# Kernel optimization log

Measured on AMD Instinct MI355X. Metric: run time of the kernel, lower is better.

Reference implementation:

```python
import jax, jax.numpy as jnp
import numpy as np

N, E, D, L, G = 10000, 320000, 256, 5, 128
RWSE, DEG_V = 16, 1001
BN_EPS = 1e-5


def setup_inputs() -> dict:
    key = jax.random.key(0)
    ks = jax.random.split(key, 12)
    s = 1.0 / np.sqrt(D)
    return {
        'feat_id': jax.random.randint(ks[0], (N,), 0, 100000, dtype=jnp.int64 if jax.config.jax_enable_x64 else jnp.int32),
        'edge_index': jax.random.randint(ks[1], (2, E), 0, N),
        'batch_idx': jnp.sort(jax.random.randint(ks[2], (N,), 0, G)),
        'rwse': jax.random.normal(ks[3], (N, RWSE), jnp.float32),
        'in_degrees': jax.random.randint(ks[4], (N,), 0, DEG_V),
        # value_projection: Linear(fixed_input_dim=D -> D); stored as [in, out]
        'w_val': jax.random.normal(ks[5], (D, D), jnp.float32) * s,
        'b_val': jnp.zeros((D,), jnp.float32),
        # rwse_projection: Linear(RWSE -> D)
        'w_rwse': jax.random.normal(ks[6], (RWSE, D), jnp.float32) * (1.0 / np.sqrt(RWSE)),
        'b_rwse': jnp.zeros((D,), jnp.float32),
        # degree_embedding table (clamped to [0, 1000])
        'deg_emb': jax.random.normal(ks[7], (DEG_V, D), jnp.float32) * 0.02,
        # per-layer GIN MLP: Linear-ReLU-Linear, stacked over L layers
        'mlp_w1': jax.random.normal(ks[8], (L, D, D), jnp.float32) * s,
        'mlp_b1': jnp.zeros((L, D), jnp.float32),
        'mlp_w2': jax.random.normal(ks[9], (L, D, D), jnp.float32) * s,
        'mlp_b2': jnp.zeros((L, D), jnp.float32),
        # BatchNorm1d (eval mode: running stats)
        'bn_gamma': jnp.ones((L, D), jnp.float32),
        'bn_beta': jnp.zeros((L, D), jnp.float32),
        'bn_mean': jnp.zeros((L, D), jnp.float32),
        'bn_var': jax.random.uniform(ks[10], (L, D), jnp.float32, 0.5, 1.5),
        # GIN eps per layer
        'eps_gin': jnp.zeros((L,), jnp.float32),
    }


def reference(feat_id, edge_index, batch_idx, rwse, in_degrees,
              w_val, b_val, w_rwse, b_rwse, deg_emb,
              mlp_w1, mlp_b1, mlp_w2, mlp_b2,
              bn_gamma, bn_beta, bn_mean, bn_var, eps_gin):
    # --- node feature embedding ---
    h_id = jnp.remainder(feat_id, D)
    h_one = jax.nn.one_hot(h_id, D, dtype=jnp.float32)            # [N, D]
    h = h_one @ w_val + b_val + rwse @ w_rwse + b_rwse            # value + rwse projections
    deg = jnp.clip(in_degrees, 0, 1000)
    h = h + deg_emb[deg]                                          # degree embedding

    src, dst = edge_index[0], edge_index[1]
    for l in range(L):
        # GIN message passing: sum neighbor features into dst (gather -> scatter-add)
        agg = jax.ops.segment_sum(h[src], dst, num_segments=N)    # [N, D]
        y = agg + (1.0 + eps_gin[l]) * h
        # MLP (Linear-ReLU-Linear)
        y = jax.nn.relu(y @ mlp_w1[l] + mlp_b1[l]) @ mlp_w2[l] + mlp_b2[l]
        # BatchNorm1d (eval: running stats) + ReLU
        y = (y - bn_mean[l]) * (bn_gamma[l] * jax.lax.rsqrt(bn_var[l] + BN_EPS)) + bn_beta[l]
        h = jax.nn.relu(y)

    # --- mean pooling per graph ---
    sums = jax.ops.segment_sum(h, batch_idx, num_segments=G)                     # [G, D]
    cnt = jax.ops.segment_sum(jnp.ones((N, 1), h.dtype), batch_idx, num_segments=G)
    graph_feature = sums / jnp.maximum(cnt, 1.0)
    return graph_feature, h
```

## Files before the change

kernel.cpp:

```cpp
#include <hip/hip_runtime.h>
#include <hip/hip_bf16.h>

#define N_NODES 10000
#define N_EDGES 320000
#define DIM     256
#define N_LAYERS 5
#define N_GRAPHS 128
#define RWSE_K  16
#define GBM 16

typedef __bf16 bf16_t;
typedef bf16_t bf16x8 __attribute__((ext_vector_type(8)));
typedef float  f32x4  __attribute__((ext_vector_type(4)));

__device__ inline ushort f2bf(float f) {
    union { float f; unsigned u; } v; v.f = f;
    unsigned r = v.u + 0x7fff + ((v.u >> 16) & 1);
    return (ushort)(r >> 16);
}
__device__ inline float bfbits2f(unsigned hi16) {
    union { unsigned u; float f; } v; v.u = hi16;
    return v.f;
}

__global__ __launch_bounds__(256)
void setup_kernel(const int* __restrict__ feat_id,
                  const float* __restrict__ rwse,
                  const int* __restrict__ in_deg,
                  const float* __restrict__ w_val,
                  const float* __restrict__ b_val,
                  const float* __restrict__ w_rwse,
                  const float* __restrict__ b_rwse,
                  const float* __restrict__ deg_emb,
                  ushort* __restrict__ hb,
                  const int* __restrict__ ei, int* __restrict__ cnt_arr,
                  const float* __restrict__ w1, const float* __restrict__ w2,
                  ushort* __restrict__ wt1, ushort* __restrict__ wt2,
                  const float* __restrict__ gamma, const float* __restrict__ beta,
                  const float* __restrict__ mean, const float* __restrict__ var,
                  const float* __restrict__ b2, float* __restrict__ scale,
                  float* __restrict__ shift) {
    __shared__ float r[RWSE_K];
    __shared__ float t[32][33];
    int b = blockIdx.x;
    int tid = threadIdx.x;
    if (b < N_NODES) {
        int i = b, d = tid;
        if (d < RWSE_K) r[d] = rwse[i * RWSE_K + d];
        __syncthreads();
        int hid = feat_id[i] & (DIM - 1);
        int dg = in_deg[i];
        dg = dg < 0 ? 0 : (dg > 1000 ? 1000 : dg);
        float v = w_val[hid * DIM + d] + b_val[d] + b_rwse[d] + deg_emb[dg * DIM + d];
#pragma unroll
        for (int k = 0; k < RWSE_K; ++k) v += r[k] * w_rwse[k * DIM + d];
        hb[i * DIM + d] = f2bf(v);
    } else if (b < 11250) {
        int e = (b - N_NODES) * 256 + tid;
        if (e < N_EDGES) atomicAdd(&cnt_arr[ei[N_EDGES + e]], 1);
    } else if (b < 11890) {
        int w_id = b - 11250;
        int l = w_id >> 7;
        int rem = w_id & 127;
        int mat = rem >> 6;
        int tile = rem & 63;
        const float* W  = (mat ? w2  : w1)  + (size_t)l * DIM * DIM;
        ushort*      Wt = (mat ? wt2 : wt1) + (size_t)l * DIM * DIM;
        int k0 = (tile >> 3) * 32, n0 = (tile & 7) * 32;
        int tx = tid & 31, ty = tid >> 5;
#pragma unroll
        for (int j = 0; j < 4; ++j)
            t[ty + j * 8][tx] = W[(k0 + ty + j * 8) * DIM + n0 + tx];
        __syncthreads();
#pragma unroll
        for (int j = 0; j < 4; ++j)
            Wt[(n0 + ty + j * 8) * DIM + k0 + tx] = f2bf(t[tx][ty + j * 8]);
    } else {
        int l = b - 11890;
        int idx = l * DIM + tid;
        float s = gamma[idx] * rsqrtf(var[idx] + 1e-5f);
        scale[idx] = s;
        shift[idx] = beta[idx] + (b2[idx] - mean[idx]) * s;
    }
}

__global__ __launch_bounds__(1024)
void scan_kernel(const int* __restrict__ cnt_arr, int* __restrict__ cur, int n) {
    __shared__ int wsum[16];
    __shared__ int carry_sh;
    int tid = threadIdx.x, wave = tid >> 6, lane = tid & 63;
    if (tid == 0) carry_sh = 0;
    __syncthreads();
    for (int base = 0; base < n; base += 1024) {
        int idx = base + tid;
        int v = (idx < n) ? cnt_arr[idx] : 0;
        int s = v;
#pragma unroll
        for (int off = 1; off < 64; off <<= 1) {
            int t = __shfl_up(s, off, 64);
            if (lane >= off) s += t;
        }
        if (lane == 63) wsum[wave] = s;
        __syncthreads();
        if (wave == 0) {
            int ws = (lane < 16) ? wsum[lane] : 0;
#pragma unroll
            for (int off = 1; off < 16; off <<= 1) {
                int t = __shfl_up(ws, off, 64);
                if (lane >= off) ws += t;
            }
            if (lane < 16) wsum[lane] = ws;
        }
        __syncthreads();
        int excl = s - v + (wave ? wsum[wave - 1] : 0) + carry_sh;
        if (idx < n) cur[idx] = excl;
        __syncthreads();
        if (tid == 0) carry_sh += wsum[15];
        __syncthreads();
    }
}

__global__ __launch_bounds__(256)
void fill_kernel(const int* __restrict__ ei, int* __restrict__ cur,
                 int* __restrict__ cs) {
    int e = blockIdx.x * 256 + threadIdx.x;
    if (e < N_EDGES) {
        int d = ei[N_EDGES + e];
        int p = atomicAdd(&cur[d], 1);
        cs[p] = ei[e];
    }
}

#define ACCV(v)                                                        \
    acc[0] += bfbits2f((v).x << 16); acc[1] += bfbits2f((v).x & 0xffff0000u); \
    acc[2] += bfbits2f((v).y << 16); acc[3] += bfbits2f((v).y & 0xffff0000u); \
    acc[4] += bfbits2f((v).z << 16); acc[5] += bfbits2f((v).z & 0xffff0000u); \
    acc[6] += bfbits2f((v).w << 16); acc[7] += bfbits2f((v).w & 0xffff0000u);

__global__ __launch_bounds__(256)
void layer_kernel(const ushort* __restrict__ hb_in,
                  const int* __restrict__ cur, const int* __restrict__ cs,
                  const float* __restrict__ eps_gin, int layer,
                  const ushort* __restrict__ Wt1, const float* __restrict__ b1,
                  const ushort* __restrict__ Wt2,
                  const float* __restrict__ bnsc, const float* __restrict__ bnsh,
                  float* __restrict__ outF, ushort* __restrict__ outB) {
    __shared__ __align__(16) ushort As[GBM][DIM + 8];
    __shared__ __align__(16) ushort Bs[DIM][40];
    __shared__ __align__(16) ushort Ts[GBM][DIM + 8];
    int tx = threadIdx.x;
    int row0 = blockIdx.x * GBM;
    int wave = tx >> 6, lane = tx & 63, quad = lane >> 4, l16 = lane & 15;
    int half = lane >> 5, sl = lane & 31;
    int wc = wave * 64;
    int srow = tx >> 2;
    int skol = (tx & 3) * 8;
    const uint4* hb4 = (const uint4*)hb_in;
    float sc = 1.0f + eps_gin[layer];

#pragma unroll
    for (int n = 0; n < 4; ++n) {
        int r = wave * 4 + n;
        int i = row0 + r;
        float acc[8];
#pragma unroll
        for (int t = 0; t < 8; ++t) acc[t] = 0.f;
        int e0 = i ? cur[i - 1] : 0;
        int e1 = cur[i];
        for (int base = e0; base < e1; base += 64) {
            int rem = e1 - base;
            int cnt = rem < 64 ? rem : 64;
            int idx = (base + lane < e1) ? cs[base + lane] : 0;
            int j = 0;
            for (; j + 8 <= cnt; j += 8) {
                int s0 = __shfl(idx, j + half, 64);
                int s1 = __shfl(idx, j + 2 + half, 64);
                int s2 = __shfl(idx, j + 4 + half, 64);
                int s3 = __shfl(idx, j + 6 + half, 64);
                uint4 v0 = hb4[(size_t)s0 * 32 + sl];
                uint4 v1 = hb4[(size_t)s1 * 32 + sl];
                uint4 v2 = hb4[(size_t)s2 * 32 + sl];
                uint4 v3 = hb4[(size_t)s3 * 32 + sl];
                ACCV(v0); ACCV(v1); ACCV(v2); ACCV(v3);
            }
            for (; j + 2 <= cnt; j += 2) {
                int s = __shfl(idx, j + half, 64);
                uint4 v = hb4[(size_t)s * 32 + sl];
                ACCV(v);
            }
            if (j < cnt) {
                int s = __shfl(idx, j, 64);
                if (half == 0) {
                    uint4 v = hb4[(size_t)s * 32 + sl];
                    ACCV(v);
                }
            }
        }
#pragma unroll
        for (int t = 0; t < 8; ++t) acc[t] += __shfl_xor(acc[t], 32, 64);
        if (half == 0) {
            uint4 sv = hb4[(size_t)i * 32 + sl];
            acc[0] += bfbits2f(sv.x << 16) * sc; acc[1] += bfbits2f(sv.x & 0xffff0000u) * sc;
            acc[2] += bfbits2f(sv.y << 16) * sc; acc[3] += bfbits2f(sv.y & 0xffff0000u) * sc;
            acc[4] += bfbits2f(sv.z << 16) * sc; acc[5] += bfbits2f(sv.z & 0xffff0000u) * sc;
            acc[6] += bfbits2f(sv.w << 16) * sc; acc[7] += bfbits2f(sv.w & 0xffff0000u) * sc;
            uint4 o;
            o.x = (uint)f2bf(acc[0]) | ((uint)f2bf(acc[1]) << 16);
            o.y = (uint)f2bf(acc[2]) | ((uint)f2bf(acc[3]) << 16);
            o.z = (uint)f2bf(acc[4]) | ((uint)f2bf(acc[5]) << 16);
            o.w = (uint)f2bf(acc[6]) | ((uint)f2bf(acc[7]) << 16);
            *(uint4*)&As[r][sl * 8] = o;
        }
    }
    __syncthreads();

    f32x4 acc4[4];
#pragma unroll
    for (int t = 0; t < 4; ++t) acc4[t] = (f32x4){0.f, 0.f, 0.f, 0.f};
    for (int k0 = 0; k0 < DIM; k0 += 32) {
#pragma unroll
        for (int j = 0; j < 4; ++j) {
            int rr = srow + 64 * j;
            *(uint4*)&Bs[rr][skol] = *(const uint4*)&Wt1[(size_t)rr * DIM + k0 + skol];
        }
        __syncthreads();
        bf16x8 af = *(const bf16x8*)&As[l16][k0 + quad * 8];
#pragma unroll
        for (int tj = 0; tj < 4; ++tj) {
            bf16x8 bfv = *(const bf16x8*)&Bs[wc + tj * 16 + l16][quad * 8];
            acc4[tj] = __builtin_amdgcn_mfma_f32_16x16x32_bf16(af, bfv, acc4[tj], 0, 0, 0);
        }
        __syncthreads();
    }
#pragma unroll
    for (int tj = 0; tj < 4; ++tj) {
        int col = wc + tj * 16 + l16;
        float bias = b1[col];
#pragma unroll
        for (int r = 0; r < 4; ++r)
            Ts[quad * 4 + r][col] = f2bf(fmaxf(acc4[tj][r] + bias, 0.f));
    }
    __syncthreads();

#pragma unroll
    for (int t = 0; t < 4; ++t) acc4[t] = (f32x4){0.f, 0.f, 0.f, 0.f};
    for (int k0 = 0; k0 < DIM; k0 += 32) {
#pragma unroll
        for (int j = 0; j < 4; ++j) {
            int rr = srow + 64 * j;
            *(uint4*)&Bs[rr][skol] = *(const uint4*)&Wt2[(size_t)rr * DIM + k0 + skol];
        }
        __syncthreads();
        bf16x8 af = *(const bf16x8*)&Ts[l16][k0 + quad * 8];
#pragma unroll
        for (int tj = 0; tj < 4; ++tj) {
            bf16x8 bfv = *(const bf16x8*)&Bs[wc + tj * 16 + l16][quad * 8];
            acc4[tj] = __builtin_amdgcn_mfma_f32_16x16x32_bf16(af, bfv, acc4[tj], 0, 0, 0);
        }
        __syncthreads();
    }
#pragma unroll
    for (int tj = 0; tj < 4; ++tj) {
        int col = wc + tj * 16 + l16;
        float s = bnsc[col], sh = bnsh[col];
#pragma unroll
        for (int r = 0; r < 4; ++r) {
            int row = row0 + quad * 4 + r;
            float v = fmaxf(acc4[tj][r] * s + sh, 0.f);
            if (outF) outF[(size_t)row * DIM + col] = v;
            if (outB) outB[(size_t)row * DIM + col] = f2bf(v);
        }
    }
}

__global__ __launch_bounds__(256)
void pool_kernel(const float* __restrict__ hfin, const int* __restrict__ batch,
                 float* __restrict__ out) {
    int g = blockIdx.x;
    int d = threadIdx.x;
    int l = 0, r = N_NODES;
    while (l < r) { int m = (l + r) >> 1; if (batch[m] < g) l = m + 1; else r = m; }
    int lo = l;
    r = N_NODES;
    while (l < r) { int m = (l + r) >> 1; if (batch[m] < g + 1) l = m + 1; else r = m; }
    int hi = l;
    float a0 = 0.f, a1 = 0.f, a2 = 0.f, a3 = 0.f;
    int i = lo;
    for (; i + 4 <= hi; i += 4) {
        a0 += hfin[(size_t)i * DIM + d];
        a1 += hfin[(size_t)(i + 1) * DIM + d];
        a2 += hfin[(size_t)(i + 2) * DIM + d];
        a3 += hfin[(size_t)(i + 3) * DIM + d];
    }
    for (; i < hi; ++i) a0 += hfin[(size_t)i * DIM + d];
    float c = (float)(hi - lo);
    if (c < 1.f) c = 1.f;
    out[g * DIM + d] = ((a0 + a1) + (a2 + a3)) / c;
}

extern "C" void kernel_launch(void* const* d_in, const int* in_sizes, int n_in,
                              void* d_out, int out_size, void* d_ws, size_t ws_size,
                              hipStream_t stream) {
    const int*   feat_id  = (const int*)d_in[0];
    const int*   ei       = (const int*)d_in[1];
    const int*   batch    = (const int*)d_in[2];
    const float* rwse     = (const float*)d_in[3];
    const int*   in_deg   = (const int*)d_in[4];
    const float* w_val    = (const float*)d_in[5];
    const float* b_val    = (const float*)d_in[6];
    const float* w_rwse   = (const float*)d_in[7];
    const float* b_rwse   = (const float*)d_in[8];
    const float* deg_emb  = (const float*)d_in[9];
    const float* mlp_w1   = (const float*)d_in[10];
    const float* mlp_b1   = (const float*)d_in[11];
    const float* mlp_w2   = (const float*)d_in[12];
    const float* mlp_b2   = (const float*)d_in[13];
    const float* bn_gamma = (const float*)d_in[14];
    const float* bn_beta  = (const float*)d_in[15];
    const float* bn_mean  = (const float*)d_in[16];
    const float* bn_var   = (const float*)d_in[17];
    const float* eps_gin  = (const float*)d_in[18];

    float* out = (float*)d_out;
    float* out_h = out + N_GRAPHS * DIM;

    char* w = (char*)d_ws;
    ushort* hb0  = (ushort*)w;
    ushort* hb1  = hb0 + (size_t)N_NODES * DIM;
    ushort* wt1  = hb1 + (size_t)N_NODES * DIM;
    ushort* wt2  = wt1 + (size_t)N_LAYERS * DIM * DIM;
    int* cnt_arr = (int*)(wt2 + (size_t)N_LAYERS * DIM * DIM);
    int* cur     = cnt_arr + N_NODES;
    int* cs      = cur + N_NODES;
    float* bnsc  = (float*)(cs + N_EDGES);
    float* bnsh  = bnsc + N_LAYERS * DIM;

    hipMemsetAsync(cnt_arr, 0, N_NODES * sizeof(int), stream);

    setup_kernel<<<11895, 256, 0, stream>>>(
        feat_id, rwse, in_deg, w_val, b_val, w_rwse, b_rwse, deg_emb,
        hb0, ei, cnt_arr, mlp_w1, mlp_w2, wt1, wt2,
        bn_gamma, bn_beta, bn_mean, bn_var, mlp_b2, bnsc, bnsh);
    scan_kernel<<<1, 1024, 0, stream>>>(cnt_arr, cur, N_NODES);
    fill_kernel<<<(N_EDGES + 255) / 256, 256, 0, stream>>>(ei, cur, cs);

    int ggrid = N_NODES / GBM;
    for (int l = 0; l < N_LAYERS; ++l) {
        bool last = (l == N_LAYERS - 1);
        const ushort* hin = (l & 1) ? hb1 : hb0;
        ushort* hout = (l & 1) ? hb0 : hb1;
        layer_kernel<<<ggrid, 256, 0, stream>>>(
            hin, cur, cs, eps_gin, l,
            wt1 + (size_t)l * DIM * DIM, mlp_b1 + l * DIM,
            wt2 + (size_t)l * DIM * DIM, bnsc + l * DIM, bnsh + l * DIM,
            last ? out_h : nullptr, last ? nullptr : hout);
    }

    pool_kernel<<<N_GRAPHS, 256, 0, stream>>>(out_h, batch, out);
}
```

Measured before the change: 329.7 us.

## Use 512-thread blocks with two interleaved rows per wave in GIN layer gather

The layer kernel now runs with 512 threads (8 waves) per block of 16 rows. Each wave aggregates two destination rows, and the neighbour gathers for both rows are interleaved in one loop so more independent loads are in flight at once. The MFMA stage is split so each wave computes 32 output columns instead of 64, and weight tiles are staged with fewer loads per thread. This aims to hide gather latency and raise occupancy, at the cost of more complex tail handling and duplicated code paths for the two rows.

```diff
diff --git a/kernel.cpp b/kernel.cpp
--- a/kernel.cpp
+++ b/kernel.cpp
@@ -131,13 +131,38 @@
     }
 }
 
-#define ACCV(v)                                                        \
-    acc[0] += bfbits2f((v).x << 16); acc[1] += bfbits2f((v).x & 0xffff0000u); \
-    acc[2] += bfbits2f((v).y << 16); acc[3] += bfbits2f((v).y & 0xffff0000u); \
-    acc[4] += bfbits2f((v).z << 16); acc[5] += bfbits2f((v).z & 0xffff0000u); \
-    acc[6] += bfbits2f((v).w << 16); acc[7] += bfbits2f((v).w & 0xffff0000u);
-
-__global__ __launch_bounds__(256)
+#define ACCP(a, v)                                                        \
+    a[0] += bfbits2f((v).x << 16); a[1] += bfbits2f((v).x & 0xffff0000u); \
+    a[2] += bfbits2f((v).y << 16); a[3] += bfbits2f((v).y & 0xffff0000u); \
+    a[4] += bfbits2f((v).z << 16); a[5] += bfbits2f((v).z & 0xffff0000u); \
+    a[6] += bfbits2f((v).w << 16); a[7] += bfbits2f((v).w & 0xffff0000u);
+
+#define SOLO8(idx, j, cnt, a)                                   \
+    for (; j + 8 <= cnt; j += 8) {                              \
+        int s0 = __shfl(idx, j + half, 64);                     \
+        int s1 = __shfl(idx, j + 2 + half, 64);                 \
+        int s2 = __shfl(idx, j + 4 + half, 64);                 \
+        int s3 = __shfl(idx, j + 6 + half, 64);                 \
+        uint4 v0 = hb4[(size_t)s0 * 32 + sl];                   \
+        uint4 v1 = hb4[(size_t)s1 * 32 + sl];                   \
+        uint4 v2 = hb4[(size_t)s2 * 32 + sl];                   \
+        uint4 v3 = hb4[(size_t)s3 * 32 + sl];                   \
+        ACCP(a, v0); ACCP(a, v1); ACCP(a, v2); ACCP(a, v3);     \
+    }                                                           \
+    for (; j + 2 <= cnt; j += 2) {                              \
+        int s = __shfl(idx, j + half, 64);                      \
+        uint4 v = hb4[(size_t)s * 32 + sl];                     \
+        ACCP(a, v);                                             \
+    }                                                           \
+    if (j < cnt) {                                              \
+        int s = __shfl(idx, j, 64);                             \
+        if (half == 0) {                                        \
+            uint4 v = hb4[(size_t)s * 32 + sl];                 \
+            ACCP(a, v);                                         \
+        }                                                       \
+    }
+
+__global__ __launch_bounds__(512)
 void layer_kernel(const ushort* __restrict__ hb_in,
                   const int* __restrict__ cur, const int* __restrict__ cs,
                   const float* __restrict__ eps_gin, int layer,
@@ -152,89 +177,112 @@
     int row0 = blockIdx.x * GBM;
     int wave = tx >> 6, lane = tx & 63, quad = lane >> 4, l16 = lane & 15;
     int half = lane >> 5, sl = lane & 31;
-    int wc = wave * 64;
+    int wc2 = wave * 32;
     int srow = tx >> 2;
     int skol = (tx & 3) * 8;
     const uint4* hb4 = (const uint4*)hb_in;
     float sc = 1.0f + eps_gin[layer];
 
-#pragma unroll
-    for (int n = 0; n < 4; ++n) {
-        int r = wave * 4 + n;
-        int i = row0 + r;
-        float acc[8];
-#pragma unroll
-        for (int t = 0; t < 8; ++t) acc[t] = 0.f;
-        int e0 = i ? cur[i - 1] : 0;
-        int e1 = cur[i];
-        for (int base = e0; base < e1; base += 64) {
-            int rem = e1 - base;
-            int cnt = rem < 64 ? rem : 64;
-            int idx = (base + lane < e1) ? cs[base + lane] : 0;
-            int j = 0;
-            for (; j + 8 <= cnt; j += 8) {
-                int s0 = __shfl(idx, j + half, 64);
-                int s1 = __shfl(idx, j + 2 + half, 64);
-                int s2 = __shfl(idx, j + 4 + half, 64);
-                int s3 = __shfl(idx, j + 6 + half, 64);
-                uint4 v0 = hb4[(size_t)s0 * 32 + sl];
-                uint4 v1 = hb4[(size_t)s1 * 32 + sl];
-                uint4 v2 = hb4[(size_t)s2 * 32 + sl];
-                uint4 v3 = hb4[(size_t)s3 * 32 + sl];
-                ACCV(v0); ACCV(v1); ACCV(v2); ACCV(v3);
-            }
-            for (; j + 2 <= cnt; j += 2) {
-                int s = __shfl(idx, j + half, 64);
-                uint4 v = hb4[(size_t)s * 32 + sl];
-                ACCV(v);
-            }
-            if (j < cnt) {
-                int s = __shfl(idx, j, 64);
-                if (half == 0) {
-                    uint4 v = hb4[(size_t)s * 32 + sl];
-                    ACCV(v);
-                }
-            }
-        }
-#pragma unroll
-        for (int t = 0; t < 8; ++t) acc[t] += __shfl_xor(acc[t], 32, 64);
-        if (half == 0) {
-            uint4 sv = hb4[(size_t)i * 32 + sl];
-            acc[0] += bfbits2f(sv.x << 16) * sc; acc[1] += bfbits2f(sv.x & 0xffff0000u) * sc;
-            acc[2] += bfbits2f(sv.y << 16) * sc; acc[3] += bfbits2f(sv.y & 0xffff0000u) * sc;
-            acc[4] += bfbits2f(sv.z << 16) * sc; acc[5] += bfbits2f(sv.z & 0xffff0000u) * sc;
-            acc[6] += bfbits2f(sv.w << 16) * sc; acc[7] += bfbits2f(sv.w & 0xffff0000u) * sc;
-            uint4 o;
-            o.x = (uint)f2bf(acc[0]) | ((uint)f2bf(acc[1]) << 16);
-            o.y = (uint)f2bf(acc[2]) | ((uint)f2bf(acc[3]) << 16);
-            o.z = (uint)f2bf(acc[4]) | ((uint)f2bf(acc[5]) << 16);
-            o.w = (uint)f2bf(acc[6]) | ((uint)f2bf(acc[7]) << 16);
-            *(uint4*)&As[r][sl * 8] = o;
-        }
+    int iA = row0 + wave * 2;
+    int iB = iA + 1;
+    int eA0 = iA ? cur[iA - 1] : 0;
+    int eA1 = cur[iA];
+    int eB1 = cur[iB];
+    uint4 sv = hb4[(size_t)(half ? iB : iA) * 32 + sl];
+    int idxA = (eA0 + lane < eA1) ? cs[eA0 + lane] : 0;
+    int idxB = (eA1 + lane < eB1) ? cs[eA1 + lane] : 0;
+    int inA = eA1 - eA0; int cntA = inA < 64 ? inA : 64;
+    int inB = eB1 - eA1; int cntB = inB < 64 ? inB : 64;
+    float accA[8], accB[8];
+#pragma unroll
+    for (int t = 0; t < 8; ++t) { accA[t] = 0.f; accB[t] = 0.f; }
+    int jA = 0, jB = 0;
+    while (jA + 8 <= cntA && jB + 8 <= cntB) {
+        int a0 = __shfl(idxA, jA + half, 64);
+        int a1 = __shfl(idxA, jA + 2 + half, 64);
+        int a2 = __shfl(idxA, jA + 4 + half, 64);
+        int a3 = __shfl(idxA, jA + 6 + half, 64);
+        int b0 = __shfl(idxB, jB + half, 64);
+        int b1s = __shfl(idxB, jB + 2 + half, 64);
+        int b2s = __shfl(idxB, jB + 4 + half, 64);
+        int b3s = __shfl(idxB, jB + 6 + half, 64);
+        uint4 va0 = hb4[(size_t)a0 * 32 + sl];
+        uint4 va1 = hb4[(size_t)a1 * 32 + sl];
+        uint4 va2 = hb4[(size_t)a2 * 32 + sl];
+        uint4 va3 = hb4[(size_t)a3 * 32 + sl];
+        uint4 vb0 = hb4[(size_t)b0 * 32 + sl];
+        uint4 vb1 = hb4[(size_t)b1s * 32 + sl];
+        uint4 vb2 = hb4[(size_t)b2s * 32 + sl];
+        uint4 vb3 = hb4[(size_t)b3s * 32 + sl];
+        ACCP(accA, va0); ACCP(accA, va1); ACCP(accA, va2); ACCP(accA, va3);
+        ACCP(accB, vb0); ACCP(accB, vb1); ACCP(accB, vb2); ACCP(accB, vb3);
+        jA += 8; jB += 8;
+    }
+    SOLO8(idxA, jA, cntA, accA);
+    SOLO8(idxB, jB, cntB, accB);
+    for (int base = eA0 + 64; base < eA1; base += 64) {
+        int idx = (base + lane < eA1) ? cs[base + lane] : 0;
+        int rem = eA1 - base; int cnt = rem < 64 ? rem : 64;
+        int j = 0;
+        SOLO8(idx, j, cnt, accA);
+    }
+    for (int base = eA1 + 64; base < eB1; base += 64) {
+        int idx = (base + lane < eB1) ? cs[base + lane] : 0;
+        int rem = eB1 - base; int cnt = rem < 64 ? rem : 64;
+        int j = 0;
+        SOLO8(idx, j, cnt, accB);
+    }
+#pragma unroll
+    for (int t = 0; t < 8; ++t) {
+        accA[t] += __shfl_xor(accA[t], 32, 64);
+        accB[t] += __shfl_xor(accB[t], 32, 64);
+    }
+    if (half == 0) {
+        accA[0] += bfbits2f(sv.x << 16) * sc; accA[1] += bfbits2f(sv.x & 0xffff0000u) * sc;
+        accA[2] += bfbits2f(sv.y << 16) * sc; accA[3] += bfbits2f(sv.y & 0xffff0000u) * sc;
+        accA[4] += bfbits2f(sv.z << 16) * sc; accA[5] += bfbits2f(sv.z & 0xffff0000u) * sc;
+        accA[6] += bfbits2f(sv.w << 16) * sc; accA[7] += bfbits2f(sv.w & 0xffff0000u) * sc;
+        uint4 o;
+        o.x = (uint)f2bf(accA[0]) | ((uint)f2bf(accA[1]) << 16);
+        o.y = (uint)f2bf(accA[2]) | ((uint)f2bf(accA[3]) << 16);
+        o.z = (uint)f2bf(accA[4]) | ((uint)f2bf(accA[5]) << 16);
+        o.w = (uint)f2bf(accA[6]) | ((uint)f2bf(accA[7]) << 16);
+        *(uint4*)&As[wave * 2][sl * 8] = o;
+    } else {
+        accB[0] += bfbits2f(sv.x << 16) * sc; accB[1] += bfbits2f(sv.x & 0xffff0000u) * sc;
+        accB[2] += bfbits2f(sv.y << 16) * sc; accB[3] += bfbits2f(sv.y & 0xffff0000u) * sc;
+        accB[4] += bfbits2f(sv.z << 16) * sc; accB[5] += bfbits2f(sv.z & 0xffff0000u) * sc;
+        accB[6] += bfbits2f(sv.w << 16) * sc; accB[7] += bfbits2f(sv.w & 0xffff0000u) * sc;
+        uint4 o;
+        o.x = (uint)f2bf(accB[0]) | ((uint)f2bf(accB[1]) << 16);
+        o.y = (uint)f2bf(accB[2]) | ((uint)f2bf(accB[3]) << 16);
+        o.z = (uint)f2bf(accB[4]) | ((uint)f2bf(accB[5]) << 16);
+        o.w = (uint)f2bf(accB[6]) | ((uint)f2bf(accB[7]) << 16);
+        *(uint4*)&As[wave * 2 + 1][sl * 8] = o;
     }
     __syncthreads();
 
-    f32x4 acc4[4];
-#pragma unroll
-    for (int t = 0; t < 4; ++t) acc4[t] = (f32x4){0.f, 0.f, 0.f, 0.f};
+    f32x4 acc4[2];
+#pragma unroll
+    for (int t = 0; t < 2; ++t) acc4[t] = (f32x4){0.f, 0.f, 0.f, 0.f};
     for (int k0 = 0; k0 < DIM; k0 += 32) {
 #pragma unroll
-        for (int j = 0; j < 4; ++j) {
-            int rr = srow + 64 * j;
+        for (int j = 0; j < 2; ++j) {
+            int rr = srow + 128 * j;
             *(uint4*)&Bs[rr][skol] = *(const uint4*)&Wt1[(size_t)rr * DIM + k0 + skol];
         }
         __syncthreads();
         bf16x8 af = *(const bf16x8*)&As[l16][k0 + quad * 8];
 #pragma unroll
-        for (int tj = 0; tj < 4; ++tj) {
-            bf16x8 bfv = *(const bf16x8*)&Bs[wc + tj * 16 + l16][quad * 8];
+        for (int tj = 0; tj < 2; ++tj) {
+            bf16x8 bfv = *(const bf16x8*)&Bs[wc2 + tj * 16 + l16][quad * 8];
             acc4[tj] = __builtin_amdgcn_mfma_f32_16x16x32_bf16(af, bfv, acc4[tj], 0, 0, 0);
         }
         __syncthreads();
     }
 #pragma unroll
-    for (int tj = 0; tj < 4; ++tj) {
-        int col = wc + tj * 16 + l16;
+    for (int tj = 0; tj < 2; ++tj) {
+        int col = wc2 + tj * 16 + l16;
         float bias = b1[col];
 #pragma unroll
         for (int r = 0; r < 4; ++r)
@@ -243,25 +291,25 @@
     __syncthreads();
 
 #pragma unroll
-    for (int t = 0; t < 4; ++t) acc4[t] = (f32x4){0.f, 0.f, 0.f, 0.f};
+    for (int t = 0; t < 2; ++t) acc4[t] = (f32x4){0.f, 0.f, 0.f, 0.f};
     for (int k0 = 0; k0 < DIM; k0 += 32) {
 #pragma unroll
-        for (int j = 0; j < 4; ++j) {
-            int rr = srow + 64 * j;
+        for (int j = 0; j < 2; ++j) {
+            int rr = srow + 128 * j;
             *(uint4*)&Bs[rr][skol] = *(const uint4*)&Wt2[(size_t)rr * DIM + k0 + skol];
         }
         __syncthreads();
         bf16x8 af = *(const bf16x8*)&Ts[l16][k0 + quad * 8];
 #pragma unroll
-        for (int tj = 0; tj < 4; ++tj) {
-            bf16x8 bfv = *(const bf16x8*)&Bs[wc + tj * 16 + l16][quad * 8];
+        for (int tj = 0; tj < 2; ++tj) {
+            bf16x8 bfv = *(const bf16x8*)&Bs[wc2 + tj * 16 + l16][quad * 8];
             acc4[tj] = __builtin_amdgcn_mfma_f32_16x16x32_bf16(af, bfv, acc4[tj], 0, 0, 0);
         }
         __syncthreads();
     }
 #pragma unroll
-    for (int tj = 0; tj < 4; ++tj) {
-        int col = wc + tj * 16 + l16;
+    for (int tj = 0; tj < 2; ++tj) {
+        int col = wc2 + tj * 16 + l16;
         float s = bnsc[col], sh = bnsh[col];
 #pragma unroll
         for (int r = 0; r < 4; ++r) {
@@ -349,7 +397,7 @@
         bool last = (l == N_LAYERS - 1);
         const ushort* hin = (l & 1) ? hb1 : hb0;
         ushort* hout = (l & 1) ? hb0 : hb1;
-        layer_kernel<<<ggrid, 256, 0, stream>>>(
+        layer_kernel<<<ggrid, 512, 0, stream>>>(
             hin, cur, cs, eps_gin, l,
             wt1 + (size_t)l * DIM * DIM, mlp_b1 + l * DIM,
             wt2 + (size_t)l * DIM * DIM, bnsc + l * DIM, bnsh + l * DIM,
```

Result: slower. 337.4 us (+2.3%).
